# Optimization experiments

Hardware: AMD Instinct MI355X
Metric: run time of the kernel (lower is better)

Reference implementation:

```python
import jax, jax.numpy as jnp
import numpy as np
from jax import lax

AR_VOCAB = 25
EN_VOCAB = 25
N_CLASSES = 1 + AR_VOCAB + EN_VOCAB + AR_VOCAB * EN_VOCAB  # full_table id layout
NEG = -jnp.inf
BIG_NEG = -1e30  # acts as log(0) in float32 (exp underflows to exactly 0) but keeps grads finite
T_LEN = 256
V_LEN = 256


def setup_inputs() -> dict:
    key = jax.random.key(0)
    k1, k2 = jax.random.split(key)
    ar_sent = jax.random.randint(k1, (1, T_LEN), 0, AR_VOCAB)
    en_sent = jax.random.randint(k2, (1, V_LEN), 0, EN_VOCAB)
    # self.weights = log(uniform) over target classes
    weights = jnp.full((N_CLASSES,), -jnp.log(jnp.float32(N_CLASSES)), dtype=jnp.float32)
    return {"ar_sent": ar_sent, "en_sent": en_sent, "weights": weights}


def _chain(c, m):
    """Solve a[0]=c[0]; a[i]=logaddexp(c[i], m[i]+a[i-1]) in parallel.
    a[i] = s[i] + logcumsumexp(c - s)[i] with s = prefix sums of m (s[0]=0)."""
    s = jnp.concatenate([jnp.zeros((1,), c.dtype), jnp.cumsum(m[1:])])
    return s + lax.associative_scan(jnp.logaddexp, c - s)


def _safe_lse(x, axis):
    """Stable logsumexp that returns -inf (with zero gradient) on empty/-inf slices."""
    m = lax.stop_gradient(jnp.max(x, axis=axis, keepdims=True))
    m = jnp.where(jnp.isfinite(m), m, 0.0)
    s = jnp.sum(jnp.exp(x - m), axis=axis)
    ok = s > 0
    return jnp.squeeze(m, axis=axis) + jnp.where(ok, jnp.log(jnp.where(ok, s, 1.0)), NEG)


def _forward(ar, en, weights):
    # ar: [T] int, en: [V] int, weights: [C] log-probs
    T, V = ar.shape[0], en.shape[0]
    del_ids = 1 + ar                                               # [T]
    ins_ids = 1 + AR_VOCAB + en                                    # [V]
    sub_ids = 1 + AR_VOCAB + EN_VOCAB + EN_VOCAB * ar[:, None] + en[None, :]  # [T,V]
    w_del = weights[del_ids]   # [T]
    w_ins = weights[ins_ids]   # [V]
    w_sub = weights[sub_ids]   # [T,V]

    # ---- alpha DP (forward lattice) ----
    # row 0: alpha[0,0]=0, alpha[0,v]=alpha[0,v-1]+w_ins[v]
    c0 = jnp.full((V,), BIG_NEG, weights.dtype).at[0].set(0.0)
    row0 = _chain(c0, w_ins)

    def fstep(prev, xs):
        wd, ws = xs  # w_del[t] scalar, w_sub[t,:] [V]
        # c[v] = logaddexp(w_del[t]+alpha[t-1,v], w_sub[t,v]+alpha[t-1,v-1]); v=0 has no sub term
        c = jnp.concatenate([(wd + prev[0])[None],
                             jnp.logaddexp(wd + prev[1:], ws[1:] + prev[:-1])])
        row = _chain(c, w_ins)  # adds within-row insertion recurrence
        return row, row

    _, frows = lax.scan(fstep, row0, (w_del[1:], w_sub[1:]))
    alpha = jnp.concatenate([row0[None], frows], axis=0)  # [T,V]

    # ---- beta DP (backward lattice) ----
    m_rev = w_ins[::-1]
    cT = jnp.full((V,), BIG_NEG, weights.dtype).at[-1].set(0.0)
    rowT = _chain(cT[::-1], m_rev)[::-1]

    def bstep(nxt, xs):
        wd, ws = xs
        # c[v] = logaddexp(w_del[t]+beta[t+1,v], w_sub[t,v]+beta[t+1,v+1]); v=V-1 has no sub term
        c = jnp.concatenate([jnp.logaddexp(wd + nxt[:-1], ws[:-1] + nxt[1:]),
                             (wd + nxt[-1])[None]])
        row = _chain(c[::-1], m_rev)[::-1]  # beta[t,v] += w_ins[v]+beta[t,v+1] recurrence
        return row, row

    _, brows = lax.scan(bstep, rowT, (w_del[:-1], w_sub[:-1]), reverse=True)
    beta = jnp.concatenate([brows, rowT[None]], axis=0)  # [T,V]

    # ---- expected edit-operation counts (log space) ----
    cls = jnp.arange(N_CLASSES)
    w = weights[None, None, :]
    md = jnp.where(del_ids[1:, None, None] == cls, 0.0, NEG)   # [T-1,1,C] one-hot log mask
    mi = jnp.where(ins_ids[None, 1:, None] == cls, 0.0, NEG)   # [1,V-1,C]
    ms = jnp.where(sub_ids[1:, 1:, None] == cls, 0.0, NEG)     # [T-1,V-1,C]
    ed = alpha[:-1, :, None] + w + md + beta[1:, :, None]      # expected deletions
    ei = alpha[:, :-1, None] + w + mi + beta[:, 1:, None]      # expected insertions
    es = alpha[:-1, :-1, None] + w + ms + beta[1:, 1:, None]   # expected substitutions
    return _safe_lse(jnp.stack([_safe_lse(ed, (0, 1)),
                                _safe_lse(ei, (0, 1)),
                                _safe_lse(es, (0, 1))]), 0)    # [C]


def reference(ar_sent, en_sent, weights):
    return _forward(ar_sent[0], en_sent[0], weights)
```

## Files before the change

kernel.cpp:

```cpp
#include <hip/hip_runtime.h>
#include <math.h>

#define NCLS 676
#define NEG_SENTINEL -3.0e38f
#define LN2F 0.6931471805599453f
#define JPAD 768
#define RS 256
#define QIP_OFF 692
#define WSE_OFF (QIP_OFF + JPAD)
#define SHM_FLOATS (WSE_OFF + 25 * JPAD + 32)
#define MAGIC 0x13579BDFu
#define NSLICE 8

__device__ __forceinline__ float dpp_shr1(float x) {
  return __int_as_float(
      __builtin_amdgcn_update_dpp(0, __float_as_int(x), 0x138, 0xF, 0xF, false));
}
__device__ __forceinline__ float dpp_shl1(float x) {
  return __int_as_float(
      __builtin_amdgcn_update_dpp(0, __float_as_int(x), 0x130, 0xF, 0xF, false));
}
__device__ __forceinline__ int dpp_shr1_i(int x) {
  return __builtin_amdgcn_update_dpp(0, x, 0x138, 0xF, 0xF, false);
}
__device__ __forceinline__ int dpp_shl1_i(int x) {
  return __builtin_amdgcn_update_dpp(0, x, 0x130, 0xF, 0xF, false);
}
__device__ __forceinline__ float pow2c(int d) {
  d = min(max(d, -126), 126);
  return __int_as_float((d + 127) << 23);
}

__global__ __launch_bounds__(256, 1) void k_dp(const int* __restrict__ ar,
                                               const int* __restrict__ en,
                                               const float* __restrict__ wts,
                                               float* __restrict__ aD,
                                               float* __restrict__ bD,
                                               int* __restrict__ aEb,
                                               int* __restrict__ bEb,
                                               float* __restrict__ S,
                                               unsigned* __restrict__ flags) {
  const int tid = threadIdx.x;
  __shared__ alignas(16) float shm[SHM_FLOATS + 4];

  if (blockIdx.x >= 2) {
    int* ctl = (int*)shm;
    if (tid == 0) ctl[0] = 0;
    __syncthreads();
    if (tid == 0) {
      while (__hip_atomic_load(&flags[0], __ATOMIC_RELAXED,
                               __HIP_MEMORY_SCOPE_AGENT) != MAGIC ||
             __hip_atomic_load(&flags[1], __ATOMIC_RELAXED,
                               __HIP_MEMORY_SCOPE_AGENT) != MAGIC)
        __builtin_amdgcn_s_sleep(16);
      __hip_atomic_store(&ctl[0], 1, __ATOMIC_RELEASE,
                         __HIP_MEMORY_SCOPE_WORKGROUP);
    } else if (tid >= 64) {
      float x = 1.0f + (float)tid;
      while (__hip_atomic_load(&ctl[0], __ATOMIC_RELAXED,
                               __HIP_MEMORY_SCOPE_WORKGROUP) == 0) {
#pragma unroll
        for (int z = 0; z < 128; ++z) x = fmaf(x, 1.0000001f, 1.0e-7f);
      }
      if (x == 123.456f) atomicAdd(&S[0], 0.f);
    }
    return;
  }

  float* pw = shm;
  float* qip = shm + QIP_OFF;
  float* wsE = shm + WSE_OFF;
  int* dctl = (int*)(shm + SHM_FLOATS);
  for (int c = tid; c < NCLS; c += 256) pw[c] = __expf(wts[c]);
  {
    float4* z = (float4*)(shm + NCLS);
    const int nz = (SHM_FLOATS - NCLS) / 4;
    for (int t = tid; t < nz; t += 256) z[t] = make_float4(0.f, 0.f, 0.f, 0.f);
  }
  if (tid == 0) *dctl = 0;
  if (blockIdx.x == 0) {
    for (int c = tid; c < NSLICE * NCLS; c += 256) S[c] = 0.f;
    if (tid == 0)
      __hip_atomic_store(&flags[2], 0u, __ATOMIC_RELAXED,
                         __HIP_MEMORY_SCOPE_AGENT);
  }
  __syncthreads();
  {
    int j = tid;
    int ee = en[j];
    qip[255 + j] = pw[26 + ee];
#pragma unroll
    for (int a = 0; a < 25; ++a) wsE[a * JPAD + 255 + j] = pw[51 + 25 * a + ee];
  }
  __syncthreads();
  if (tid >= 64) {
    float x = 1.0f + (float)tid;
    while (__hip_atomic_load(dctl, __ATOMIC_RELAXED,
                             __HIP_MEMORY_SCOPE_WORKGROUP) == 0) {
#pragma unroll
      for (int z = 0; z < 128; ++z) x = fmaf(x, 1.0000001f, 1.0e-7f);
    }
    if (x == 123.456f) atomicAdd(&S[0], 0.f);
    return;
  }
  const int lane = tid;

  const int i0 = 4 * lane;
  float wdl[4];
  const float* rowp[4];
#pragma unroll
  for (int k = 0; k < 4; ++k) {
    int a = ar[i0 + k];
    wdl[k] = pw[1 + a];
    rowp[k] = wsE + a * JPAD;
  }
  float P1[4] = {0.f, 0.f, 0.f, 0.f};
  float P2[4] = {0.f, 0.f, 0.f, 0.f};
  int e1 = 0;

  if (blockIdx.x == 0) {
    if (lane == 0) { P1[0] = 1.f; aD[255] = 1.f; }
    int e0 = 252 - i0;
    float* sp = aD + RS + 252 - i0;
    int* ep = aEb + lane;
    float W[4][12], Q[12];

#define LOAD_A(EB, W, Q)                                                   \
  {                                                                        \
    _Pragma("unroll") for (int k = 0; k < 4; ++k) {                        \
      const float4* p = (const float4*)(rowp[k] + (EB));                   \
      float4 va = p[0], vb = p[1], vc = p[2];                              \
      W[k][0] = va.x; W[k][1] = va.y; W[k][2] = va.z; W[k][3] = va.w;      \
      W[k][4] = vb.x; W[k][5] = vb.y; W[k][6] = vb.z; W[k][7] = vb.w;      \
      W[k][8] = vc.x; W[k][9] = vc.y; W[k][10] = vc.z; W[k][11] = vc.w;    \
    }                                                                      \
    const float4* q = (const float4*)(qip + (EB));                         \
    float4 qa = q[0], qb = q[1], qc = q[2];                                \
    Q[0] = qa.x; Q[1] = qa.y; Q[2] = qa.z; Q[3] = qa.w;                    \
    Q[4] = qb.x; Q[5] = qb.y; Q[6] = qb.z; Q[7] = qb.w;                    \
    Q[8] = qc.x; Q[9] = qc.y; Q[10] = qc.z; Q[11] = qc.w;                  \
  }

    LOAD_A(e0, W, Q);
    for (int pr = 0; pr < 64; ++pr) {
      const int e1st = e1;
      int t1e = dpp_shr1_i(e1);
      float f1n = pow2c(t1e - e1);
      float pmc = dpp_shr1(P2[3]) * f1n;
      float cs[8][4];
#pragma unroll
      for (int u = 0; u < 8; ++u) {
        float pm1 = dpp_shr1(P1[3]) * f1n;
        float pm2 = pmc;
#pragma unroll
        for (int k = 0; k < 4; ++k) {
          float a1 = (k == 0) ? pm1 : P1[k - 1];
          float a2 = (k == 0) ? pm2 : P2[k - 1];
          cs[u][k] = fmaf(wdl[k], a1,
                          fmaf(W[k][4 + u - k], a2, Q[4 + u - k] * P1[k]));
        }
#pragma unroll
        for (int k = 0; k < 4; ++k) {
          P2[k] = P1[k]; P1[k] = cs[u][k];
        }
        pmc = pm1;
      }
#pragma unroll
      for (int u = 0; u < 8; ++u) {
        *(float4*)sp = make_float4(cs[u][3], cs[u][2], cs[u][1], cs[u][0]);
        sp += RS;
      }
      e0 += 8;
      LOAD_A(e0, W, Q);
      float m = fmaxf(fmaxf(P1[0], P1[1]), fmaxf(P1[2], P1[3]));
      int ex = (m > 0.f) ? ((__float_as_int(m) >> 23) - 126) : (t1e - e1);
      float sc = pow2c(-ex);
#pragma unroll
      for (int k = 0; k < 4; ++k) {
        P1[k] *= sc; P2[k] *= sc;
      }
      e1 += ex;
      *ep = e1st; ep += 64;
    }
  } else {
    if (lane == 63) P1[3] = 1.f;
    if (lane == 0) bD[510 * RS] = 1.f;
    int e0 = 764 - i0;
    float* sp = bD + 509 * RS + 252 - i0;
    int* ep = bEb + lane;
    float W[4][16], Q[16];

#define LOAD_B(EB, W, Q)                                                   \
  {                                                                        \
    _Pragma("unroll") for (int k = 0; k < 4; ++k) {                        \
      const float4* p = (const float4*)(rowp[k] + (EB));                   \
      float4 va = p[0], vb = p[1], vc = p[2], vd = p[3];                   \
      W[k][0] = va.x; W[k][1] = va.y; W[k][2] = va.z; W[k][3] = va.w;      \
      W[k][4] = vb.x; W[k][5] = vb.y; W[k][6] = vb.z; W[k][7] = vb.w;      \
      W[k][8] = vc.x; W[k][9] = vc.y; W[k][10] = vc.z; W[k][11] = vc.w;    \
      W[k][12] = vd.x; W[k][13] = vd.y; W[k][14] = vd.z; W[k][15] = vd.w;  \
    }                                                                      \
    const float4* q = (const float4*)(qip + (EB));                         \
    float4 qa = q[0], qb = q[1], qc = q[2], qd = q[3];                     \
    Q[0] = qa.x; Q[1] = qa.y; Q[2] = qa.z; Q[3] = qa.w;                    \
    Q[4] = qb.x; Q[5] = qb.y; Q[6] = qb.z; Q[7] = qb.w;                    \
    Q[8] = qc.x; Q[9] = qc.y; Q[10] = qc.z; Q[11] = qc.w;                  \
    Q[12] = qd.x; Q[13] = qd.y; Q[14] = qd.z; Q[15] = qd.w;                \
  }

    LOAD_B(e0, W, Q);
    for (int pr = 0; pr < 64; ++pr) {
      const int e1st = e1;
      int t1e = dpp_shl1_i(e1);
      float f1n = pow2c(t1e - e1);
      float pmc = dpp_shl1(P2[0]) * f1n;
      float cs[8][4];
#pragma unroll
      for (int u = 0; u < 8; ++u) {
        float pm1 = dpp_shl1(P1[0]) * f1n;
        float pm2 = pmc;
#pragma unroll
        for (int k = 0; k < 4; ++k) {
          float a1 = (k == 3) ? pm1 : P1[k + 1];
          float a2 = (k == 3) ? pm2 : P2[k + 1];
          cs[u][k] = fmaf(wdl[k], a1,
                          fmaf(W[k][12 - u - k], a2, Q[13 - u - k] * P1[k]));
        }
#pragma unroll
        for (int k = 0; k < 4; ++k) {
          P2[k] = P1[k]; P1[k] = cs[u][k];
        }
        pmc = pm1;
      }
#pragma unroll
      for (int u = 0; u < 8; ++u) {
        *(float4*)sp = make_float4(cs[u][3], cs[u][2], cs[u][1], cs[u][0]);
        sp -= RS;
      }
      e0 -= 8;
      LOAD_B(e0, W, Q);
      float m = fmaxf(fmaxf(P1[0], P1[1]), fmaxf(P1[2], P1[3]));
      int ex = (m > 0.f) ? ((__float_as_int(m) >> 23) - 126) : (t1e - e1);
      float sc = pow2c(-ex);
#pragma unroll
      for (int k = 0; k < 4; ++k) {
        P1[k] *= sc; P2[k] *= sc;
      }
      e1 += ex;
      *ep = e1st; ep += 64;
    }
  }

  __hip_atomic_store(dctl, 1, __ATOMIC_RELEASE, __HIP_MEMORY_SCOPE_WORKGROUP);
  __threadfence();
  if (lane == 0)
    __hip_atomic_store(&flags[blockIdx.x], MAGIC, __ATOMIC_RELEASE,
                       __HIP_MEMORY_SCOPE_AGENT);
}

__global__ __launch_bounds__(256) void k_red(const int* __restrict__ ar,
                                             const int* __restrict__ en,
                                             const float* __restrict__ wts,
                                             const float* __restrict__ aD,
                                             const float* __restrict__ bD,
                                             const int* __restrict__ aEb,
                                             const int* __restrict__ bEb,
                                             float* __restrict__ S,
                                             unsigned* __restrict__ flags,
                                             float* __restrict__ out) {
  const int tid = threadIdx.x;
  __shared__ float bins[NCLS];
  __shared__ int ctl;
  for (int c = tid; c < NCLS; c += 256) bins[c] = 0.f;
  __syncthreads();
  const float M = __logf(aD[510 * RS]) +
                  (float)aEb[63 * 64 + 63] * LN2F + 16.0f;
  const int j = tid;
  const int e = en[j];
#pragma unroll
  for (int u = 0; u < 4; ++u) {
    const int d = (int)blockIdx.x * 4 + u;
    if (d <= 510) {
      const int i = d - j;
      if (i >= 0 && i <= 255) {
        const float bM = bD[d * RS + 255 - i];
        if (bM > 0.f) {
          const int bEx =
              (d == 510) ? 0 : bEb[((509 - d) >> 3) * 64 + (i >> 2)];
          const float lb = __logf(bM) + (float)bEx * LN2F - M;
          const int a = ar[i];
          if (i >= 1) {
            float aM = aD[(d - 1) * RS + 256 - i];
            if (aM > 0.f) {
              int eA = (d == 1) ? 0 : aEb[((d - 2) >> 3) * 64 + ((i - 1) >> 2)];
              float L = __logf(aM) + (float)eA * LN2F + lb;
              atomicAdd(&bins[1 + a], __expf(fminf(L, 0.f)));
            }
          }
          if (j >= 1) {
            float aM = aD[(d - 1) * RS + 255 - i];
            if (aM > 0.f) {
              int eA = (d == 1) ? 0 : aEb[((d - 2) >> 3) * 64 + (i >> 2)];
              float L = __logf(aM) + (float)eA * LN2F + lb;
              atomicAdd(&bins[26 + e], __expf(fminf(L, 0.f)));
            }
            if (i >= 1) {
              float aM2 = aD[(d - 2) * RS + 256 - i];
              if (aM2 > 0.f) {
                int eA2 =
                    (d == 2) ? 0 : aEb[((d - 3) >> 3) * 64 + ((i - 1) >> 2)];
                float L2 = __logf(aM2) + (float)eA2 * LN2F + lb;
                atomicAdd(&bins[51 + 25 * a + e], __expf(fminf(L2, 0.f)));
              }
            }
          }
        }
      }
    }
  }
  __syncthreads();
  float* Ss = S + (blockIdx.x & (NSLICE - 1)) * NCLS;
  for (int c = tid; c < NCLS; c += 256)
    if (bins[c] != 0.f) atomicAdd(&Ss[c], bins[c]);
  __syncthreads();
  if (tid == 0) {
    unsigned n = __hip_atomic_fetch_add(&flags[2], 1u, __ATOMIC_ACQ_REL,
                                        __HIP_MEMORY_SCOPE_AGENT);
    ctl = ((n & 127u) == 127u);
  }
  __syncthreads();
  if (ctl) {
    for (int c = tid; c < NCLS; c += 256) {
      float s = 0.f;
#pragma unroll
      for (int q = 0; q < NSLICE; ++q)
        s += __hip_atomic_load(&S[q * NCLS + c], __ATOMIC_RELAXED,
                               __HIP_MEMORY_SCOPE_AGENT);
      out[c] = (c != 0 && s > 0.f) ? (wts[c] + M + __logf(s)) : NEG_SENTINEL;
    }
  }
}

extern "C" void kernel_launch(void* const* d_in, const int* in_sizes, int n_in,
                              void* d_out, int out_size, void* d_ws, size_t ws_size,
                              hipStream_t stream) {
  const int* ar = (const int*)d_in[0];
  const int* en = (const int*)d_in[1];
  const float* wts = (const float*)d_in[2];
  float* aD = (float*)d_ws;
  float* bDraw = aD + 514 * RS;
  float* bD = bDraw + 2 * RS;
  int* aEb = (int*)(bDraw + 514 * RS);
  int* bEb = aEb + 4096;
  float* S = (float*)(bEb + 4096);
  unsigned* flags = (unsigned*)(S + NSLICE * NCLS);
  k_dp<<<130, 256, 0, stream>>>(ar, en, wts, aD, bD, aEb, bEb, S, flags);
  k_red<<<128, 256, 0, stream>>>(ar, en, wts, aD, bD, aEb, bEb, S, flags,
                                 (float*)d_out);
}
```

Baseline: 96.64 us.

## Split each DP chain across two wavefronts with an LDS producer-consumer handoff

Each alpha and beta wavefront DP is now split across two wavefronts that each own 2 rows per lane, down from 4. The upstream wave passes its boundary values and exponents through a double-buffered LDS slot, with progress and consume counters for flow control. This halves the serial per-lane FMA chain and aims to cut latency on the critical path. The costs are spin-wait synchronisation between the waves and a larger per-row exponent table (256 entries per block of rows), which the reduction kernel indexes accordingly.

```diff
diff --git a/kernel.cpp b/kernel.cpp
--- a/kernel.cpp
+++ b/kernel.cpp
@@ -8,7 +8,12 @@
 #define RS 256
 #define QIP_OFF 692
 #define WSE_OFF (QIP_OFF + JPAD)
-#define SHM_FLOATS (WSE_OFF + 25 * JPAD + 32)
+#define TBL_END (WSE_OFF + 25 * JPAD + 32)
+#define CTL_PROG 20692
+#define CTL_CONS 20693
+#define CTL_DCTL 20694
+#define SLOT_OFF 20696
+#define SHM_TOT 20720
 #define MAGIC 0x13579BDFu
 #define NSLICE 8
 
@@ -41,7 +46,7 @@
                                                float* __restrict__ S,
                                                unsigned* __restrict__ flags) {
   const int tid = threadIdx.x;
-  __shared__ alignas(16) float shm[SHM_FLOATS + 4];
+  __shared__ alignas(16) float shm[SHM_TOT];
 
   if (blockIdx.x >= 2) {
     int* ctl = (int*)shm;
@@ -70,14 +75,17 @@
   float* pw = shm;
   float* qip = shm + QIP_OFF;
   float* wsE = shm + WSE_OFF;
-  int* dctl = (int*)(shm + SHM_FLOATS);
+  int* progp = (int*)(shm + CTL_PROG);
+  int* consp = (int*)(shm + CTL_CONS);
+  int* dctlp = (int*)(shm + CTL_DCTL);
+  float* slotp = shm + SLOT_OFF;
   for (int c = tid; c < NCLS; c += 256) pw[c] = __expf(wts[c]);
   {
     float4* z = (float4*)(shm + NCLS);
-    const int nz = (SHM_FLOATS - NCLS) / 4;
+    const int nz = (SHM_TOT - NCLS) / 4;
     for (int t = tid; t < nz; t += 256) z[t] = make_float4(0.f, 0.f, 0.f, 0.f);
   }
-  if (tid == 0) *dctl = 0;
+  if (tid == 0) { *progp = 0; *consp = 0; *dctlp = 0; }
   if (blockIdx.x == 0) {
     for (int c = tid; c < NSLICE * NCLS; c += 256) S[c] = 0.f;
     if (tid == 0)
@@ -93,9 +101,11 @@
     for (int a = 0; a < 25; ++a) wsE[a * JPAD + 255 + j] = pw[51 + 25 * a + ee];
   }
   __syncthreads();
-  if (tid >= 64) {
+  const int wid = tid >> 6;
+  const int lane = tid & 63;
+  if (wid >= 2) {
     float x = 1.0f + (float)tid;
-    while (__hip_atomic_load(dctl, __ATOMIC_RELAXED,
+    while (__hip_atomic_load(dctlp, __ATOMIC_RELAXED,
                              __HIP_MEMORY_SCOPE_WORKGROUP) == 0) {
 #pragma unroll
       for (int z = 0; z < 128; ++z) x = fmaf(x, 1.0000001f, 1.0e-7f);
@@ -103,159 +113,286 @@
     if (x == 123.456f) atomicAdd(&S[0], 0.f);
     return;
   }
-  const int lane = tid;
-
-  const int i0 = 4 * lane;
-  float wdl[4];
-  const float* rowp[4];
-#pragma unroll
-  for (int k = 0; k < 4; ++k) {
+
+  const int i0 = 2 * lane + 128 * wid;
+  float wdl[2];
+  const float* rowp[2];
+#pragma unroll
+  for (int k = 0; k < 2; ++k) {
     int a = ar[i0 + k];
     wdl[k] = pw[1 + a];
     rowp[k] = wsE + a * JPAD;
   }
-  float P1[4] = {0.f, 0.f, 0.f, 0.f};
-  float P2[4] = {0.f, 0.f, 0.f, 0.f};
+  float P1[2] = {0.f, 0.f};
+  float P2[2] = {0.f, 0.f};
   int e1 = 0;
 
+#define LOAD_A2(EB)                                                        \
+  {                                                                        \
+    _Pragma("unroll") for (int k = 0; k < 2; ++k) {                        \
+      const float2* p2 = (const float2*)(rowp[k] + (EB));                  \
+      float2 va = p2[0], vb = p2[1], vc = p2[2], vd = p2[3], ve = p2[4],   \
+             vf = p2[5];                                                   \
+      W[k][0] = va.x; W[k][1] = va.y; W[k][2] = vb.x; W[k][3] = vb.y;      \
+      W[k][4] = vc.x; W[k][5] = vc.y; W[k][6] = vd.x; W[k][7] = vd.y;      \
+      W[k][8] = ve.x; W[k][9] = ve.y; W[k][10] = vf.x; W[k][11] = vf.y;    \
+    }                                                                      \
+    const float2* q2 = (const float2*)(qip + (EB));                        \
+    float2 qa = q2[0], qb = q2[1], qc = q2[2], qd = q2[3], qe = q2[4],     \
+           qf = q2[5];                                                     \
+    Q[0] = qa.x; Q[1] = qa.y; Q[2] = qb.x; Q[3] = qb.y; Q[4] = qc.x;       \
+    Q[5] = qc.y; Q[6] = qd.x; Q[7] = qd.y; Q[8] = qe.x; Q[9] = qe.y;       \
+    Q[10] = qf.x; Q[11] = qf.y;                                            \
+  }
+
+#define LOAD_B2(EB)                                                        \
+  {                                                                        \
+    _Pragma("unroll") for (int k = 0; k < 2; ++k) {                        \
+      const float2* p2 = (const float2*)(rowp[k] + (EB));                  \
+      float2 va = p2[0], vb = p2[1], vc = p2[2], vd = p2[3], ve = p2[4],   \
+             vf = p2[5], vg = p2[6], vh = p2[7];                           \
+      W[k][0] = va.x; W[k][1] = va.y; W[k][2] = vb.x; W[k][3] = vb.y;      \
+      W[k][4] = vc.x; W[k][5] = vc.y; W[k][6] = vd.x; W[k][7] = vd.y;      \
+      W[k][8] = ve.x; W[k][9] = ve.y; W[k][10] = vf.x; W[k][11] = vf.y;    \
+      W[k][12] = vg.x; W[k][13] = vg.y; W[k][14] = vh.x; W[k][15] = vh.y;  \
+    }                                                                      \
+    const float2* q2 = (const float2*)(qip + (EB));                        \
+    float2 qa = q2[0], qb = q2[1], qc = q2[2], qd = q2[3], qe = q2[4],     \
+           qf = q2[5], qg = q2[6], qh = q2[7];                             \
+    Q[0] = qa.x; Q[1] = qa.y; Q[2] = qb.x; Q[3] = qb.y; Q[4] = qc.x;       \
+    Q[5] = qc.y; Q[6] = qd.x; Q[7] = qd.y; Q[8] = qe.x; Q[9] = qe.y;       \
+    Q[10] = qf.x; Q[11] = qf.y; Q[12] = qg.x; Q[13] = qg.y; Q[14] = qh.x;  \
+    Q[15] = qh.y;                                                          \
+  }
+
   if (blockIdx.x == 0) {
-    if (lane == 0) { P1[0] = 1.f; aD[255] = 1.f; }
-    int e0 = 252 - i0;
-    float* sp = aD + RS + 252 - i0;
-    int* ep = aEb + lane;
-    float W[4][12], Q[12];
-
-#define LOAD_A(EB, W, Q)                                                   \
-  {                                                                        \
-    _Pragma("unroll") for (int k = 0; k < 4; ++k) {                        \
-      const float4* p = (const float4*)(rowp[k] + (EB));                   \
-      float4 va = p[0], vb = p[1], vc = p[2];                              \
-      W[k][0] = va.x; W[k][1] = va.y; W[k][2] = va.z; W[k][3] = va.w;      \
-      W[k][4] = vb.x; W[k][5] = vb.y; W[k][6] = vb.z; W[k][7] = vb.w;      \
-      W[k][8] = vc.x; W[k][9] = vc.y; W[k][10] = vc.z; W[k][11] = vc.w;    \
-    }                                                                      \
-    const float4* q = (const float4*)(qip + (EB));                         \
-    float4 qa = q[0], qb = q[1], qc = q[2];                                \
-    Q[0] = qa.x; Q[1] = qa.y; Q[2] = qa.z; Q[3] = qa.w;                    \
-    Q[4] = qb.x; Q[5] = qb.y; Q[6] = qb.z; Q[7] = qb.w;                    \
-    Q[8] = qc.x; Q[9] = qc.y; Q[10] = qc.z; Q[11] = qc.w;                  \
-  }
-
-    LOAD_A(e0, W, Q);
-    for (int pr = 0; pr < 64; ++pr) {
-      const int e1st = e1;
-      int t1e = dpp_shr1_i(e1);
-      float f1n = pow2c(t1e - e1);
-      float pmc = dpp_shr1(P2[3]) * f1n;
-      float cs[8][4];
-#pragma unroll
-      for (int u = 0; u < 8; ++u) {
-        float pm1 = dpp_shr1(P1[3]) * f1n;
-        float pm2 = pmc;
-#pragma unroll
-        for (int k = 0; k < 4; ++k) {
-          float a1 = (k == 0) ? pm1 : P1[k - 1];
-          float a2 = (k == 0) ? pm2 : P2[k - 1];
-          cs[u][k] = fmaf(wdl[k], a1,
-                          fmaf(W[k][4 + u - k], a2, Q[4 + u - k] * P1[k]));
-        }
-#pragma unroll
-        for (int k = 0; k < 4; ++k) {
-          P2[k] = P1[k]; P1[k] = cs[u][k];
-        }
-        pmc = pm1;
-      }
-#pragma unroll
-      for (int u = 0; u < 8; ++u) {
-        *(float4*)sp = make_float4(cs[u][3], cs[u][2], cs[u][1], cs[u][0]);
-        sp += RS;
-      }
-      e0 += 8;
-      LOAD_A(e0, W, Q);
-      float m = fmaxf(fmaxf(P1[0], P1[1]), fmaxf(P1[2], P1[3]));
-      int ex = (m > 0.f) ? ((__float_as_int(m) >> 23) - 126) : (t1e - e1);
-      float sc = pow2c(-ex);
-#pragma unroll
-      for (int k = 0; k < 4; ++k) {
-        P1[k] *= sc; P2[k] *= sc;
-      }
-      e1 += ex;
-      *ep = e1st; ep += 64;
+    if (wid == 0) {
+      if (lane == 0) { P1[0] = 1.f; aD[255] = 1.f; }
+      int e0 = 252 - i0;
+      float* sp = aD + RS + 254 - i0;
+      int* ep = aEb + i0;
+      float W[2][12], Q[12];
+      LOAD_A2(e0);
+      for (int p = 0; p < 64; ++p) {
+        const int e1st = e1;
+        int t1e = dpp_shr1_i(e1);
+        float f1n = pow2c(t1e - e1);
+        float pmc = dpp_shr1(P2[1]) * f1n;
+        float cs[8][2];
+#pragma unroll
+        for (int u = 0; u < 8; ++u) {
+          float pm1 = dpp_shr1(P1[1]) * f1n;
+          float pm2 = pmc;
+          float c0 = fmaf(wdl[0], pm1, fmaf(W[0][4 + u], pm2, Q[4 + u] * P1[0]));
+          float c1 = fmaf(wdl[1], P1[0], fmaf(W[1][3 + u], P2[0], Q[3 + u] * P1[1]));
+          cs[u][0] = c0; cs[u][1] = c1;
+          P2[0] = P1[0]; P2[1] = P1[1]; P1[0] = c0; P1[1] = c1;
+          pmc = pm1;
+        }
+        if (lane == 63) {
+          while (__hip_atomic_load(consp, __ATOMIC_RELAXED,
+                                   __HIP_MEMORY_SCOPE_WORKGROUP) < p - 1) {}
+          float* sl = slotp + (p & 1) * 12;
+          *(float4*)(sl) = make_float4(cs[0][1], cs[1][1], cs[2][1], cs[3][1]);
+          *(float4*)(sl + 4) = make_float4(cs[4][1], cs[5][1], cs[6][1], cs[7][1]);
+          ((int*)sl)[8] = e1st;
+          __hip_atomic_store(progp, p + 1, __ATOMIC_RELEASE,
+                             __HIP_MEMORY_SCOPE_WORKGROUP);
+        }
+#pragma unroll
+        for (int u = 0; u < 8; ++u) {
+          *(float2*)sp = make_float2(cs[u][1], cs[u][0]);
+          sp += RS;
+        }
+        e0 += 8;
+        LOAD_A2(e0);
+        float m = fmaxf(P1[0], P1[1]);
+        int ex = (m > 0.f) ? ((__float_as_int(m) >> 23) - 126) : (t1e - e1);
+        float sc = pow2c(-ex);
+        P1[0] *= sc; P1[1] *= sc; P2[0] *= sc; P2[1] *= sc;
+        e1 += ex;
+        *(int2*)ep = make_int2(e1st, e1st); ep += 256;
+      }
+    } else {
+      int e0 = 252 - i0;
+      float* sp = aD + RS + 254 - i0;
+      int* ep = aEb + i0;
+      float W[2][12], Q[12];
+      LOAD_A2(e0);
+      float t1raw = 0.f, t2raw = 0.f;
+      int eBprev = 0;
+      const bool isL0 = (lane == 0);
+      for (int p = 0; p < 64; ++p) {
+        while (__hip_atomic_load(progp, __ATOMIC_ACQUIRE,
+                                 __HIP_MEMORY_SCOPE_WORKGROUP) < p + 1) {}
+        const float* sl = slotp + (p & 1) * 12;
+        float4 r0 = *(const float4*)sl;
+        float4 r1 = *(const float4*)(sl + 4);
+        int eB = ((const int*)sl)[8];
+        float scm = isL0 ? pow2c(eB - e1) : 0.f;
+        float spm = isL0 ? pow2c(eBprev - e1) : 0.f;
+        float B1[8];
+        B1[0] = t1raw * spm;
+        B1[1] = r0.x * scm; B1[2] = r0.y * scm; B1[3] = r0.z * scm;
+        B1[4] = r0.w * scm; B1[5] = r1.x * scm; B1[6] = r1.y * scm;
+        B1[7] = r1.z * scm;
+        float B2s = t2raw * spm;
+        t1raw = r1.w; t2raw = r1.z; eBprev = eB;
+        const int e1st = e1;
+        int td = dpp_shr1_i(e1);
+        int t1e = isL0 ? eB : td;
+        float f1n = pow2c(t1e - e1);
+        float pmc = fmaf(dpp_shr1(P2[1]), f1n, B2s);
+        float cs[8][2];
+#pragma unroll
+        for (int u = 0; u < 8; ++u) {
+          float pm1 = fmaf(dpp_shr1(P1[1]), f1n, B1[u]);
+          float pm2 = pmc;
+          float c0 = fmaf(wdl[0], pm1, fmaf(W[0][4 + u], pm2, Q[4 + u] * P1[0]));
+          float c1 = fmaf(wdl[1], P1[0], fmaf(W[1][3 + u], P2[0], Q[3 + u] * P1[1]));
+          cs[u][0] = c0; cs[u][1] = c1;
+          P2[0] = P1[0]; P2[1] = P1[1]; P1[0] = c0; P1[1] = c1;
+          pmc = pm1;
+        }
+#pragma unroll
+        for (int u = 0; u < 8; ++u) {
+          *(float2*)sp = make_float2(cs[u][1], cs[u][0]);
+          sp += RS;
+        }
+        e0 += 8;
+        LOAD_A2(e0);
+        float m = fmaxf(P1[0], P1[1]);
+        int ex = (m > 0.f) ? ((__float_as_int(m) >> 23) - 126) : (t1e - e1);
+        float sc = pow2c(-ex);
+        P1[0] *= sc; P1[1] *= sc; P2[0] *= sc; P2[1] *= sc;
+        e1 += ex;
+        *(int2*)ep = make_int2(e1st, e1st); ep += 256;
+        if (isL0)
+          __hip_atomic_store(consp, p + 1, __ATOMIC_RELEASE,
+                             __HIP_MEMORY_SCOPE_WORKGROUP);
+      }
+      __hip_atomic_store(dctlp, 1, __ATOMIC_RELEASE,
+                         __HIP_MEMORY_SCOPE_WORKGROUP);
+      __threadfence();
+      if (lane == 0)
+        __hip_atomic_store(&flags[0], MAGIC, __ATOMIC_RELEASE,
+                           __HIP_MEMORY_SCOPE_AGENT);
     }
   } else {
-    if (lane == 63) P1[3] = 1.f;
-    if (lane == 0) bD[510 * RS] = 1.f;
-    int e0 = 764 - i0;
-    float* sp = bD + 509 * RS + 252 - i0;
-    int* ep = bEb + lane;
-    float W[4][16], Q[16];
-
-#define LOAD_B(EB, W, Q)                                                   \
-  {                                                                        \
-    _Pragma("unroll") for (int k = 0; k < 4; ++k) {                        \
-      const float4* p = (const float4*)(rowp[k] + (EB));                   \
-      float4 va = p[0], vb = p[1], vc = p[2], vd = p[3];                   \
-      W[k][0] = va.x; W[k][1] = va.y; W[k][2] = va.z; W[k][3] = va.w;      \
-      W[k][4] = vb.x; W[k][5] = vb.y; W[k][6] = vb.z; W[k][7] = vb.w;      \
-      W[k][8] = vc.x; W[k][9] = vc.y; W[k][10] = vc.z; W[k][11] = vc.w;    \
-      W[k][12] = vd.x; W[k][13] = vd.y; W[k][14] = vd.z; W[k][15] = vd.w;  \
-    }                                                                      \
-    const float4* q = (const float4*)(qip + (EB));                         \
-    float4 qa = q[0], qb = q[1], qc = q[2], qd = q[3];                     \
-    Q[0] = qa.x; Q[1] = qa.y; Q[2] = qa.z; Q[3] = qa.w;                    \
-    Q[4] = qb.x; Q[5] = qb.y; Q[6] = qb.z; Q[7] = qb.w;                    \
-    Q[8] = qc.x; Q[9] = qc.y; Q[10] = qc.z; Q[11] = qc.w;                  \
-    Q[12] = qd.x; Q[13] = qd.y; Q[14] = qd.z; Q[15] = qd.w;                \
-  }
-
-    LOAD_B(e0, W, Q);
-    for (int pr = 0; pr < 64; ++pr) {
-      const int e1st = e1;
-      int t1e = dpp_shl1_i(e1);
-      float f1n = pow2c(t1e - e1);
-      float pmc = dpp_shl1(P2[0]) * f1n;
-      float cs[8][4];
-#pragma unroll
-      for (int u = 0; u < 8; ++u) {
-        float pm1 = dpp_shl1(P1[0]) * f1n;
-        float pm2 = pmc;
-#pragma unroll
-        for (int k = 0; k < 4; ++k) {
-          float a1 = (k == 3) ? pm1 : P1[k + 1];
-          float a2 = (k == 3) ? pm2 : P2[k + 1];
-          cs[u][k] = fmaf(wdl[k], a1,
-                          fmaf(W[k][12 - u - k], a2, Q[13 - u - k] * P1[k]));
-        }
-#pragma unroll
-        for (int k = 0; k < 4; ++k) {
-          P2[k] = P1[k]; P1[k] = cs[u][k];
-        }
-        pmc = pm1;
-      }
-#pragma unroll
-      for (int u = 0; u < 8; ++u) {
-        *(float4*)sp = make_float4(cs[u][3], cs[u][2], cs[u][1], cs[u][0]);
-        sp -= RS;
-      }
-      e0 -= 8;
-      LOAD_B(e0, W, Q);
-      float m = fmaxf(fmaxf(P1[0], P1[1]), fmaxf(P1[2], P1[3]));
-      int ex = (m > 0.f) ? ((__float_as_int(m) >> 23) - 126) : (t1e - e1);
-      float sc = pow2c(-ex);
-#pragma unroll
-      for (int k = 0; k < 4; ++k) {
-        P1[k] *= sc; P2[k] *= sc;
-      }
-      e1 += ex;
-      *ep = e1st; ep += 64;
-    }
-  }
-
-  __hip_atomic_store(dctl, 1, __ATOMIC_RELEASE, __HIP_MEMORY_SCOPE_WORKGROUP);
-  __threadfence();
-  if (lane == 0)
-    __hip_atomic_store(&flags[blockIdx.x], MAGIC, __ATOMIC_RELEASE,
-                       __HIP_MEMORY_SCOPE_AGENT);
+    if (wid == 1) {
+      if (lane == 63) P1[1] = 1.f;
+      if (lane == 0) bD[510 * RS] = 1.f;
+      int e0 = 764 - i0;
+      float* sp = bD + 509 * RS + 254 - i0;
+      int* ep = bEb + i0;
+      float W[2][16], Q[16];
+      LOAD_B2(e0);
+      for (int p = 0; p < 64; ++p) {
+        const int e1st = e1;
+        int t1e = dpp_shl1_i(e1);
+        float f1n = pow2c(t1e - e1);
+        float pmc = dpp_shl1(P2[0]) * f1n;
+        float cs[8][2];
+#pragma unroll
+        for (int u = 0; u < 8; ++u) {
+          float pm1 = dpp_shl1(P1[0]) * f1n;
+          float pm2 = pmc;
+          float c1 = fmaf(wdl[1], pm1, fmaf(W[1][11 - u], pm2, Q[12 - u] * P1[1]));
+          float c0 = fmaf(wdl[0], P1[1], fmaf(W[0][12 - u], P2[1], Q[13 - u] * P1[0]));
+          cs[u][0] = c0; cs[u][1] = c1;
+          P2[0] = P1[0]; P2[1] = P1[1]; P1[0] = c0; P1[1] = c1;
+          pmc = pm1;
+        }
+        if (lane == 0) {
+          while (__hip_atomic_load(consp, __ATOMIC_RELAXED,
+                                   __HIP_MEMORY_SCOPE_WORKGROUP) < p - 1) {}
+          float* sl = slotp + (p & 1) * 12;
+          *(float4*)(sl) = make_float4(cs[0][0], cs[1][0], cs[2][0], cs[3][0]);
+          *(float4*)(sl + 4) = make_float4(cs[4][0], cs[5][0], cs[6][0], cs[7][0]);
+          ((int*)sl)[8] = e1st;
+          __hip_atomic_store(progp, p + 1, __ATOMIC_RELEASE,
+                             __HIP_MEMORY_SCOPE_WORKGROUP);
+        }
+#pragma unroll
+        for (int u = 0; u < 8; ++u) {
+          *(float2*)sp = make_float2(cs[u][1], cs[u][0]);
+          sp -= RS;
+        }
+        e0 -= 8;
+        LOAD_B2(e0);
+        float m = fmaxf(P1[0], P1[1]);
+        int ex = (m > 0.f) ? ((__float_as_int(m) >> 23) - 126) : (t1e - e1);
+        float sc = pow2c(-ex);
+        P1[0] *= sc; P1[1] *= sc; P2[0] *= sc; P2[1] *= sc;
+        e1 += ex;
+        *(int2*)ep = make_int2(e1st, e1st); ep += 256;
+      }
+    } else {
+      int e0 = 764 - i0;
+      float* sp = bD + 509 * RS + 254 - i0;
+      int* ep = bEb + i0;
+      float W[2][16], Q[16];
+      LOAD_B2(e0);
+      float t1raw = 0.f, t2raw = 0.f;
+      int eBprev = 0;
+      const bool isT = (lane == 63);
+      for (int p = 0; p < 64; ++p) {
+        while (__hip_atomic_load(progp, __ATOMIC_ACQUIRE,
+                                 __HIP_MEMORY_SCOPE_WORKGROUP) < p + 1) {}
+        const float* sl = slotp + (p & 1) * 12;
+        float4 r0 = *(const float4*)sl;
+        float4 r1 = *(const float4*)(sl + 4);
+        int eB = ((const int*)sl)[8];
+        float scm = isT ? pow2c(eB - e1) : 0.f;
+        float spm = isT ? pow2c(eBprev - e1) : 0.f;
+        float B1[8];
+        B1[0] = t1raw * spm;
+        B1[1] = r0.x * scm; B1[2] = r0.y * scm; B1[3] = r0.z * scm;
+        B1[4] = r0.w * scm; B1[5] = r1.x * scm; B1[6] = r1.y * scm;
+        B1[7] = r1.z * scm;
+        float B2s = t2raw * spm;
+        t1raw = r1.w; t2raw = r1.z; eBprev = eB;
+        const int e1st = e1;
+        int td = dpp_shl1_i(e1);
+        int t1e = isT ? eB : td;
+        float f1n = pow2c(t1e - e1);
+        float pmc = fmaf(dpp_shl1(P2[0]), f1n, B2s);
+        float cs[8][2];
+#pragma unroll
+        for (int u = 0; u < 8; ++u) {
+          float pm1 = fmaf(dpp_shl1(P1[0]), f1n, B1[u]);
+          float pm2 = pmc;
+          float c1 = fmaf(wdl[1], pm1, fmaf(W[1][11 - u], pm2, Q[12 - u] * P1[1]));
+          float c0 = fmaf(wdl[0], P1[1], fmaf(W[0][12 - u], P2[1], Q[13 - u] * P1[0]));
+          cs[u][0] = c0; cs[u][1] = c1;
+          P2[0] = P1[0]; P2[1] = P1[1]; P1[0] = c0; P1[1] = c1;
+          pmc = pm1;
+        }
+#pragma unroll
+        for (int u = 0; u < 8; ++u) {
+          *(float2*)sp = make_float2(cs[u][1], cs[u][0]);
+          sp -= RS;
+        }
+        e0 -= 8;
+        LOAD_B2(e0);
+        float m = fmaxf(P1[0], P1[1]);
+        int ex = (m > 0.f) ? ((__float_as_int(m) >> 23) - 126) : (t1e - e1);
+        float sc = pow2c(-ex);
+        P1[0] *= sc; P1[1] *= sc; P2[0] *= sc; P2[1] *= sc;
+        e1 += ex;
+        *(int2*)ep = make_int2(e1st, e1st); ep += 256;
+        if (isT)
+          __hip_atomic_store(consp, p + 1, __ATOMIC_RELEASE,
+                             __HIP_MEMORY_SCOPE_WORKGROUP);
+      }
+      __hip_atomic_store(dctlp, 1, __ATOMIC_RELEASE,
+                         __HIP_MEMORY_SCOPE_WORKGROUP);
+      __threadfence();
+      if (lane == 0)
+        __hip_atomic_store(&flags[1], MAGIC, __ATOMIC_RELEASE,
+                           __HIP_MEMORY_SCOPE_AGENT);
+    }
+  }
 }
 
 __global__ __launch_bounds__(256) void k_red(const int* __restrict__ ar,
@@ -274,7 +411,7 @@
   for (int c = tid; c < NCLS; c += 256) bins[c] = 0.f;
   __syncthreads();
   const float M = __logf(aD[510 * RS]) +
-                  (float)aEb[63 * 64 + 63] * LN2F + 16.0f;
+                  (float)aEb[63 * 256 + 255] * LN2F + 16.0f;
   const int j = tid;
   const int e = en[j];
 #pragma unroll
@@ -286,13 +423,13 @@
         const float bM = bD[d * RS + 255 - i];
         if (bM > 0.f) {
           const int bEx =
-              (d == 510) ? 0 : bEb[((509 - d) >> 3) * 64 + (i >> 2)];
+              (d == 510) ? 0 : bEb[((509 - d) >> 3) * 256 + i];
           const float lb = __logf(bM) + (float)bEx * LN2F - M;
           const int a = ar[i];
           if (i >= 1) {
             float aM = aD[(d - 1) * RS + 256 - i];
             if (aM > 0.f) {
-              int eA = (d == 1) ? 0 : aEb[((d - 2) >> 3) * 64 + ((i - 1) >> 2)];
+              int eA = (d == 1) ? 0 : aEb[((d - 2) >> 3) * 256 + (i - 1)];
               float L = __logf(aM) + (float)eA * LN2F + lb;
               atomicAdd(&bins[1 + a], __expf(fminf(L, 0.f)));
             }
@@ -300,15 +437,14 @@
           if (j >= 1) {
             float aM = aD[(d - 1) * RS + 255 - i];
             if (aM > 0.f) {
-              int eA = (d == 1) ? 0 : aEb[((d - 2) >> 3) * 64 + (i >> 2)];
+              int eA = (d == 1) ? 0 : aEb[((d - 2) >> 3) * 256 + i];
               float L = __logf(aM) + (float)eA * LN2F + lb;
               atomicAdd(&bins[26 + e], __expf(fminf(L, 0.f)));
             }
             if (i >= 1) {
               float aM2 = aD[(d - 2) * RS + 256 - i];
               if (aM2 > 0.f) {
-                int eA2 =
-                    (d == 2) ? 0 : aEb[((d - 3) >> 3) * 64 + ((i - 1) >> 2)];
+                int eA2 = (d == 2) ? 0 : aEb[((d - 3) >> 3) * 256 + (i - 1)];
                 float L2 = __logf(aM2) + (float)eA2 * LN2F + lb;
                 atomicAdd(&bins[51 + 25 * a + e], __expf(fminf(L2, 0.f)));
               }
@@ -351,8 +487,8 @@
   float* bDraw = aD + 514 * RS;
   float* bD = bDraw + 2 * RS;
   int* aEb = (int*)(bDraw + 514 * RS);
-  int* bEb = aEb + 4096;
-  float* S = (float*)(bEb + 4096);
+  int* bEb = aEb + 64 * 256;
+  float* S = (float*)(bEb + 64 * 256);
   unsigned* flags = (unsigned*)(S + NSLICE * NCLS);
   k_dp<<<130, 256, 0, stream>>>(ar, en, wts, aD, bD, aEb, bEb, S, flags);
   k_red<<<128, 256, 0, stream>>>(ar, en, wts, aD, bD, aEb, bEb, S, flags,
```

Result: slower. 101.2 us (+4.8%).
